# Kernel tuning notes

Measured on AMD Instinct MI355X. Metric: run time of the kernel, lower is better.

The kernel has to match this reference:

```python
import jax, jax.numpy as jnp
import numpy as np

N = 8192       # nodes
E = 262144     # edges per graph view (avg degree 32)
D_IN = 200     # input feature dim
D = 100        # hidden dim
H = 2          # GAT heads (concat=False -> mean over heads)
K = 25         # nearest_neighbor in DHGLayer
A_H = 50       # Attention module hidden dim
LRELU = 0.2
BN_EPS = 1e-5


def _bn_eval(x, gamma, beta):
    # BatchNorm1d in eval mode with running_mean=0, running_var=1 (as initialized)
    return x * (gamma / jnp.sqrt(1.0 + BN_EPS)) + beta


def _gat(x, src, dst, W, att_src, att_dst, bias):
    # PyG GATConv: heads=H, concat=False (head mean), self-loops added, eval (no dropout)
    n = x.shape[0]
    xp = (x @ W).reshape(n, H, D)                          # (n, H, D)
    loop = jnp.arange(n, dtype=src.dtype)
    s = jnp.concatenate([src, loop])
    d = jnp.concatenate([dst, loop])
    a_s = jnp.einsum('nhc,hc->nh', xp, att_src)
    a_d = jnp.einsum('nhc,hc->nh', xp, att_dst)
    e = jax.nn.leaky_relu(a_s[s] + a_d[d], LRELU)          # (E+n, H)
    m = jax.ops.segment_max(e, d, num_segments=n)
    w = jnp.exp(e - m[d])
    z = jax.ops.segment_sum(w, d, num_segments=n)
    alpha = w / z[d]
    out = jax.ops.segment_sum(alpha[:, :, None] * xp[s], d, num_segments=n)
    return out.mean(axis=1) + bias                          # (n, D)


def _dhg(x, Wkk, bkk, w1, b1, fcW, fcb):
    # DHGLayer at ite=1: only the kNN hyperedge branch is active
    # (wu_knn=1 <= ite < wu_kmeans=2 = wu_struct=2). EdgeConv over a single
    # hyperedge degenerates to identity (softmax over one element).
    nrm = jnp.maximum(jnp.linalg.norm(x, axis=1, keepdims=True), 1e-12)
    xn = x / nrm
    sim = jax.lax.stop_gradient(xn @ xn.T)                 # cosine sim, used only for topk indices
    _, idx = jax.lax.top_k(sim, K)                         # (n, K)
    region = x[idx]                                        # (n, K, D) gather
    # Transform: grouped Conv1d(K, K*K, D) -> per-node KxK mixing weights -> softmax -> mix
    mult = jax.nn.softmax(jnp.einsum('nkd,kjd->nkj', region, Wkk) + bkk, axis=-1)
    tf = jnp.einsum('nkj,njd->nkd', mult, region)          # (n, K, D)
    pooled = jnp.einsum('nkd,k->nd', tf, w1) + b1          # Conv1d(K, 1, 1) pooling
    return jax.nn.relu(pooled @ fcW + fcb)                 # GraphConvolution fc + ReLU


def _atten(x, W1, b1, g, b, W2, b2):
    h = jax.nn.sigmoid(_bn_eval(x @ W1 + b1, g, b))
    return h @ W2 + b2                                     # (n, 1)


def _encoder(inputx, edge_index, fea_edge_index,
             g1_W, g1_as, g1_ad, g1_b, g2_W, g2_as, g2_ad, g2_b,
             g3_W, g3_as, g3_ad, g3_b, g4_W, g4_as, g4_ad, g4_b,
             bn_g, bn_b, bn1_g, bn1_b,
             d1_Wkk, d1_bkk, d1_w1, d1_b1, d1_fcW, d1_fcb,
             d2_Wkk, d2_bkk, d2_w1, d2_b1, d2_fcW, d2_fcb,
             a1_W1, a1_b1, a1_g, a1_bb, a1_W2, a1_b2,
             a2_W1, a2_b1, a2_g, a2_bb, a2_W2, a2_b2):
    fs, fd = fea_edge_index[0], fea_edge_index[1]
    es, ed = edge_index[0], edge_index[1]
    feax1 = jax.nn.relu(_bn_eval(_gat(inputx, fs, fd, g1_W, g1_as, g1_ad, g1_b), bn_g, bn_b))
    x1 = jax.nn.relu(_bn_eval(_gat(inputx, es, ed, g2_W, g2_as, g2_ad, g2_b), bn1_g, bn1_b))
    feax1 = _dhg(feax1, d1_Wkk, d1_bkk, d1_w1, d1_b1, d1_fcW, d1_fcb)
    feax2 = _gat(feax1, fs, fd, g3_W, g3_as, g3_ad, g3_b)
    x1 = _dhg(x1, d2_Wkk, d2_bkk, d2_w1, d2_b1, d2_fcW, d2_fcb)
    x2 = _gat(x1, es, ed, g4_W, g4_as, g4_ad, g4_b)
    att1 = _atten(feax2, a1_W1, a1_b1, a1_g, a1_bb, a1_W2, a1_b2)
    att2 = _atten(x2, a2_W1, a2_b1, a2_g, a2_bb, a2_W2, a2_b2)
    att = jax.nn.softmax(jnp.concatenate([att1, att2], axis=1), axis=1)
    return att[:, :1] * feax2 + att[:, 1:] * x2            # (N, D)


def setup_inputs() -> dict:
    key = jax.random.key(0)
    kit = iter(jax.random.split(key, 64))
    nrm = lambda shape, scale: jax.random.normal(next(kit), shape, dtype=jnp.float32) * scale
    inp = {}
    inp['inputx'] = nrm((N, D_IN), 1.0)
    inp['edge_index'] = jax.random.randint(next(kit), (2, E), 0, N)
    inp['fea_edge_index'] = jax.random.randint(next(kit), (2, E), 0, N)
    inp['edge_list'] = jax.random.randint(next(kit), (N, K), 0, N)  # unused at ite=1
    for name, din in (('g1', D_IN), ('g2', D_IN), ('g3', D), ('g4', D)):
        inp[name + '_W'] = nrm((din, H * D), din ** -0.5)
        inp[name + '_as'] = nrm((H, D), D ** -0.5)
        inp[name + '_ad'] = nrm((H, D), D ** -0.5)
        inp[name + '_b'] = jnp.zeros((D,), jnp.float32)
    inp['bn_g'] = jnp.ones((D,), jnp.float32)
    inp['bn_b'] = jnp.zeros((D,), jnp.float32)
    inp['bn1_g'] = jnp.ones((D,), jnp.float32)
    inp['bn1_b'] = jnp.zeros((D,), jnp.float32)
    for name in ('d1', 'd2'):
        inp[name + '_Wkk'] = nrm((K, K, D), D ** -0.5)
        inp[name + '_bkk'] = jnp.zeros((K, K), jnp.float32)
        inp[name + '_w1'] = nrm((K,), K ** -0.5)
        inp[name + '_b1'] = jnp.zeros((1,), jnp.float32)
        inp[name + '_fcW'] = nrm((D, D), D ** -0.5)
        inp[name + '_fcb'] = jnp.zeros((D,), jnp.float32)
    for name in ('a1', 'a2'):
        inp[name + '_W1'] = nrm((D, A_H), D ** -0.5)
        inp[name + '_b1'] = jnp.zeros((A_H,), jnp.float32)
        inp[name + '_g'] = jnp.ones((A_H,), jnp.float32)
        inp[name + '_bb'] = jnp.zeros((A_H,), jnp.float32)
        inp[name + '_W2'] = nrm((A_H, 1), A_H ** -0.5)
        inp[name + '_b2'] = jnp.zeros((1,), jnp.float32)
    return inp


def reference(inputx, edge_index, fea_edge_index, edge_list,
              g1_W, g1_as, g1_ad, g1_b, g2_W, g2_as, g2_ad, g2_b,
              g3_W, g3_as, g3_ad, g3_b, g4_W, g4_as, g4_ad, g4_b,
              bn_g, bn_b, bn1_g, bn1_b,
              d1_Wkk, d1_bkk, d1_w1, d1_b1, d1_fcW, d1_fcb,
              d2_Wkk, d2_bkk, d2_w1, d2_b1, d2_fcW, d2_fcb,
              a1_W1, a1_b1, a1_g, a1_bb, a1_W2, a1_b2,
              a2_W1, a2_b1, a2_g, a2_bb, a2_W2, a2_b2):
    # edge_list is ignored: structured-neighbor branch is not warmed up at ite=1
    return _encoder(inputx, edge_index, fea_edge_index,
                    g1_W, g1_as, g1_ad, g1_b, g2_W, g2_as, g2_ad, g2_b,
                    g3_W, g3_as, g3_ad, g3_b, g4_W, g4_as, g4_ad, g4_b,
                    bn_g, bn_b, bn1_g, bn1_b,
                    d1_Wkk, d1_bkk, d1_w1, d1_b1, d1_fcW, d1_fcb,
                    d2_Wkk, d2_bkk, d2_w1, d2_b1, d2_fcW, d2_fcb,
                    a1_W1, a1_b1, a1_g, a1_bb, a1_W2, a1_b2,
                    a2_W1, a2_b1, a2_g, a2_bb, a2_W2, a2_b2)
```

## Files before the change

### kernel.cpp

```cpp
#include <hip/hip_runtime.h>
#include <math.h>

#define NN 8192
#define EE 262144
#define KNN 25
#define INIT_COLS 1024
#define CAP 768
#define INF INFINITY

typedef unsigned int u32;
typedef unsigned long long u64;

__device__ __forceinline__ float lrelu02(float x){ return x > 0.f ? x : 0.2f*x; }
__device__ __forceinline__ u32 fkey(float f){ u32 b = __float_as_uint(f); return b ^ (u32)(((int)b >> 31) | (int)0x80000000); }

__global__ __launch_bounds__(256) void k_count(const int* __restrict__ dst, int* __restrict__ deg) {
  int e = blockIdx.x*256 + threadIdx.x;
  if (e < EE) atomicAdd(&deg[dst[e]], 1);
}

__global__ __launch_bounds__(1024) void k_scan(const int* __restrict__ deg, int* __restrict__ rowptr) {
  __shared__ int lds[1024];
  int t = threadIdx.x;
  int v[8]; int s = 0;
#pragma unroll
  for (int i=0;i<8;i++){ v[i] = deg[t*8+i]; s += v[i]; }
  lds[t] = s; __syncthreads();
  for (int off=1; off<1024; off<<=1) {
    int x = (t>=off)? lds[t-off] : 0;
    __syncthreads();
    lds[t] += x;
    __syncthreads();
  }
  int base = (t==0)? 0 : lds[t-1];
  if (t==0) rowptr[0] = 0;
  int run = base;
#pragma unroll
  for (int i=0;i<8;i++){ run += v[i]; rowptr[t*8+i+1] = run; }
}

__global__ __launch_bounds__(256) void k_scatter(const int* __restrict__ src, const int* __restrict__ dst,
                          const int* __restrict__ rowptr, int* __restrict__ cursor,
                          int* __restrict__ csr) {
  int e = blockIdx.x*256 + threadIdx.x;
  if (e < EE) {
    int d = dst[e];
    int p = rowptr[d] + atomicAdd(&cursor[d], 1);
    csr[p] = src[e];
  }
}

__global__ __launch_bounds__(256) void k_gemm_small(const float* __restrict__ A, const float* __restrict__ B,
                                                    float* __restrict__ C, int Ncols, int Kdim) {
  __shared__ float Al[50][65];
  __shared__ float Bl[50][65];
  int t = threadIdx.x;
  int tr = t >> 4, tc = t & 15;
  int r0 = blockIdx.x * 64, c0 = blockIdx.y * 64;
  float acc[4][4] = {};
  for (int kc = 0; kc < Kdim; kc += 50) {
    for (int fl = t; fl < 64*50; fl += 256) {
      int m = fl / 50, k = fl - m*50;
      Al[k][m] = A[(long)(r0+m)*Kdim + kc + k];
    }
    for (int fl = t; fl < 50*64; fl += 256) {
      int k = fl >> 6, c = fl & 63;
      int cg = c0 + c;
      Bl[k][c] = (cg < Ncols) ? B[(long)(kc+k)*Ncols + cg] : 0.f;
    }
    __syncthreads();
    for (int k = 0; k < 50; k++) {
      float a_[4], b_[4];
#pragma unroll
      for (int i=0;i<4;i++) a_[i] = Al[k][tr*4+i];
#pragma unroll
      for (int j=0;j<4;j++) b_[j] = Bl[k][tc*4+j];
#pragma unroll
      for (int i=0;i<4;i++)
#pragma unroll
        for (int j=0;j<4;j++) acc[i][j] += a_[i]*b_[j];
    }
    __syncthreads();
  }
#pragma unroll
  for (int i=0;i<4;i++){
    int r = r0 + tr*4 + i;
#pragma unroll
    for (int j=0;j<4;j++){
      int c = c0 + tc*4 + j;
      if (c < Ncols) C[(long)r*Ncols + c] = acc[i][j];
    }
  }
}

__global__ __launch_bounds__(256) void k_gat_coef(const float* __restrict__ xp, const float* __restrict__ as_w,
                                                  const float* __restrict__ ad_w, float* __restrict__ asb,
                                                  float* __restrict__ adb) {
  int g = blockIdx.x*256 + threadIdx.x;
  int n = g >> 2, q = g & 3;
  int h = q >> 1, sd = q & 1;
  const float4* xr = (const float4*)(xp + (long)n*200 + h*100);
  const float4* wr = (const float4*)((sd ? ad_w : as_w) + h*100);
  float acc = 0.f;
#pragma unroll
  for (int q4=0;q4<25;q4++){
    float4 xv = xr[q4], wv = wr[q4];
    acc += xv.x*wv.x + xv.y*wv.y + xv.z*wv.z + xv.w*wv.w;
  }
  (sd ? adb : asb)[n*2 + h] = acc;
}

__global__ __launch_bounds__(256) void k_gat_agg(const float* __restrict__ xp, const float* __restrict__ asb,
                                                 const float* __restrict__ adb, const int* __restrict__ rowptr,
                                                 const int* __restrict__ csr, const float* __restrict__ bias,
                                                 const float* __restrict__ bng, const float* __restrict__ bnb,
                                                 int bnrelu, float* __restrict__ out) {
  __shared__ int esrc[256];
  __shared__ float ew0[256], ew1[256];
  __shared__ float red[2][4];
  __shared__ float ohead[200];
  int i = blockIdx.x, t = threadIdx.x;
  int lane = t & 63, wv = t >> 6;
  int beg = rowptr[i];
  int deg = rowptr[i+1] - beg;
  float ad0 = adb[i*2+0], ad1 = adb[i*2+1];
  float m0 = -INF, m1 = -INF, z0 = 0.f, z1 = 0.f, acc = 0.f;
  int h = (t >= 100) ? 1 : 0;
  int tot = deg + 1;
  for (int base = 0; base < tot; base += 256) {
    int cnt = min(256, tot - base);
    int j = base + t;
    float e0 = -INF, e1 = -INF; int s = i;
    if (t < cnt) {
      if (j < deg) s = csr[beg + j];
      float as0 = asb[s*2+0], as1 = asb[s*2+1];
      e0 = lrelu02(as0 + ad0);
      e1 = lrelu02(as1 + ad1);
    }
    esrc[t] = s;
    float r0v = e0, r1v = e1;
    for (int off=32; off; off>>=1){ r0v = fmaxf(r0v, __shfl_xor(r0v,off)); r1v = fmaxf(r1v, __shfl_xor(r1v,off)); }
    if (lane == 0){ red[0][wv] = r0v; red[1][wv] = r1v; }
    __syncthreads();
    float nm0 = fmaxf(m0, fmaxf(fmaxf(red[0][0],red[0][1]), fmaxf(red[0][2],red[0][3])));
    float nm1 = fmaxf(m1, fmaxf(fmaxf(red[1][0],red[1][1]), fmaxf(red[1][2],red[1][3])));
    float w0 = (t<cnt)? expf(e0-nm0) : 0.f;
    float w1e = (t<cnt)? expf(e1-nm1) : 0.f;
    ew0[t] = w0; ew1[t] = w1e;
    float s0 = w0, s1 = w1e;
    for (int off=32; off; off>>=1){ s0 += __shfl_xor(s0,off); s1 += __shfl_xor(s1,off); }
    __syncthreads();
    if (lane == 0){ red[0][wv] = s0; red[1][wv] = s1; }
    __syncthreads();
    float cs0 = red[0][0]+red[0][1]+red[0][2]+red[0][3];
    float cs1 = red[1][0]+red[1][1]+red[1][2]+red[1][3];
    float rf0 = expf(m0 - nm0);
    float rf1 = expf(m1 - nm1);
    z0 = z0*rf0 + cs0; z1 = z1*rf1 + cs1;
    m0 = nm0; m1 = nm1;
    if (t < 200) {
      acc *= (h==0) ? rf0 : rf1;
      const float* ew = (h==0) ? ew0 : ew1;
      for (int jj = 0; jj < cnt; jj++) {
        acc += ew[jj] * xp[(long)esrc[jj]*200 + t];
      }
    }
    __syncthreads();
  }
  if (t < 200) ohead[t] = acc / ((h==0) ? z0 : z1);
  __syncthreads();
  if (t < 100) {
    float v = 0.5f*(ohead[t] + ohead[100+t]) + bias[t];
    if (bnrelu) {
      v = v * (bng[t]*rsqrtf(1.f+1e-5f)) + bnb[t];
      v = fmaxf(v, 0.f);
    }
    out[(long)i*100 + t] = v;
  }
}

__global__ __launch_bounds__(256) void k_norm(const float* __restrict__ x, float* __restrict__ xnT) {
  int w = threadIdx.x >> 6, lane = threadIdx.x & 63;
  long n = blockIdx.x*4 + w;
  float a = x[n*100 + lane];
  float b = (lane < 36) ? x[n*100 + 64 + lane] : 0.f;
  float ss = a*a + b*b;
  for (int off=32; off; off>>=1) ss += __shfl_xor(ss, off);
  float sc = 1.f / fmaxf(sqrtf(ss), 1e-12f);
  xnT[(long)lane*NN + n] = a*sc;
  if (lane < 36) xnT[(long)(64+lane)*NN + n] = b*sc;
}

__global__ __launch_bounds__(256) void k_sim(const float* __restrict__ xnT, float* __restrict__ simbuf) {
  __shared__ float Al[50][132];
  __shared__ float Bl[50][132];
  int t = threadIdx.x;
  int tr = t >> 4, tc = t & 15;
  int r0 = blockIdx.x * 128;
  int cb = blockIdx.y * 128;
  float acc[8][8] = {};
  for (int kc = 0; kc < 100; kc += 50) {
    for (int fl = t; fl < 50*128; fl += 256) {
      int k = fl >> 7, m = fl & 127;
      const float* src = xnT + (long)(kc+k)*NN;
      Al[k][m] = src[r0 + m];
      Bl[k][m] = src[cb + m];
    }
    __syncthreads();
    for (int k = 0; k < 50; k++) {
      float4 a0 = *(const float4*)&Al[k][4*tr];
      float4 a1 = *(const float4*)&Al[k][4*tr + 64];
      float4 b0 = *(const float4*)&Bl[k][4*tc];
      float4 b1 = *(const float4*)&Bl[k][4*tc + 64];
      float a_[8] = {a0.x,a0.y,a0.z,a0.w,a1.x,a1.y,a1.z,a1.w};
      float b_[8] = {b0.x,b0.y,b0.z,b0.w,b1.x,b1.y,b1.z,b1.w};
#pragma unroll
      for (int i=0;i<8;i++)
#pragma unroll
        for (int j=0;j<8;j++) acc[i][j] += a_[i]*b_[j];
    }
    __syncthreads();
  }
#pragma unroll
  for (int i=0;i<8;i++){
    long r = r0 + ((i<4) ? (4*tr + i) : (64 + 4*tr + i - 4));
    float* crow = simbuf + r*(long)INIT_COLS + cb;
    float4 o0 = make_float4(acc[i][0],acc[i][1],acc[i][2],acc[i][3]);
    float4 o1 = make_float4(acc[i][4],acc[i][5],acc[i][6],acc[i][7]);
    *(float4*)&crow[4*tc]      = o0;
    *(float4*)&crow[64 + 4*tc] = o1;
  }
}

__global__ __launch_bounds__(256) void k_sim_f(const float* __restrict__ xnT, const u32* __restrict__ thr,
                                               int* __restrict__ cnt, u64* __restrict__ candbuf, int cbase) {
  __shared__ float Al[50][132];
  __shared__ float Bl[50][132];
  int t = threadIdx.x;
  int tr = t >> 4, tc = t & 15;
  int r0 = blockIdx.x * 128;
  int cb = blockIdx.y * 128;
  float acc[8][8] = {};
  for (int kc = 0; kc < 100; kc += 50) {
    for (int fl = t; fl < 50*128; fl += 256) {
      int k = fl >> 7, m = fl & 127;
      const float* src = xnT + (long)(kc+k)*NN;
      Al[k][m] = src[r0 + m];
      Bl[k][m] = src[cbase + cb + m];
    }
    __syncthreads();
    for (int k = 0; k < 50; k++) {
      float4 a0 = *(const float4*)&Al[k][4*tr];
      float4 a1 = *(const float4*)&Al[k][4*tr + 64];
      float4 b0 = *(const float4*)&Bl[k][4*tc];
      float4 b1 = *(const float4*)&Bl[k][4*tc + 64];
      float a_[8] = {a0.x,a0.y,a0.z,a0.w,a1.x,a1.y,a1.z,a1.w};
      float b_[8] = {b0.x,b0.y,b0.z,b0.w,b1.x,b1.y,b1.z,b1.w};
#pragma unroll
      for (int i=0;i<8;i++)
#pragma unroll
        for (int j=0;j<8;j++) acc[i][j] += a_[i]*b_[j];
    }
    __syncthreads();
  }
  int sub = t & 15;
#pragma unroll
  for (int i=0;i<8;i++){
    int r = r0 + ((i<4) ? (4*tr + i) : (64 + 4*tr + i - 4));
    u32 T = thr[r];
    unsigned m8 = 0;
#pragma unroll
    for (int j=0;j<8;j++) if (fkey(acc[i][j]) > T) m8 |= 1u<<j;
    int c_lane = __popc(m8);
    int pre = c_lane;
#pragma unroll
    for (int off=1; off<16; off<<=1){ int o = __shfl_up(pre, off, 16); if (sub >= off) pre += o; }
    int tot = __shfl(pre, 15, 16);
    if (tot > 0){
      int base = 0;
      if (sub == 15) base = atomicAdd(&cnt[r], tot);
      base = __shfl(base, 15, 16);
      int p = base + pre - c_lane;
#pragma unroll
      for (int j=0;j<8;j++) if (m8 & (1u<<j)){
        if (p < CAP){
          int c = cbase + cb + ((j<4) ? (4*tc + j) : (64 + 4*tc + j - 4));
          candbuf[(long)r*CAP + p] = ((u64)fkey(acc[i][j]) << 32) | (u32)(0xFFFFFFFFu - (u32)c);
        }
        p++;
      }
    }
  }
}

__global__ __launch_bounds__(256) void k_topk_sel(const float* __restrict__ simbuf,
                                                  u64* __restrict__ candu, u32* __restrict__ thr) {
  __shared__ int hist[256];
  __shared__ int scr2[2];
  __shared__ int cgt, ceq;
  __shared__ u64 win[32];
  __shared__ u32 tie[INIT_COLS];
  int row = blockIdx.x, t = threadIdx.x, lane = t & 63, w = t >> 6;
  const float* srow = simbuf + (long)row*INIT_COLS;
  u32 kk[4]; int col[4];
  {
    int c0 = 4*t;
    float4 f = *(const float4*)&srow[c0];
    kk[0] = fkey(f.x); col[0] = c0;
    kk[1] = fkey(f.y); col[1] = c0+1;
    kk[2] = fkey(f.z); col[2] = c0+2;
    kk[3] = fkey(f.w); col[3] = c0+3;
  }
  u32 prefix = 0; int base_gt = 0;
#pragma unroll
  for (int lvl = 0; lvl < 4; lvl++) {
    int shift = 24 - 8*lvl;
    hist[t] = 0;
    if (lvl == 0 && t == 0) { cgt = 0; ceq = 0; }
    __syncthreads();
    u32 mhi = (lvl == 0) ? 0u : (0xFFFFFFFFu << (32 - 8*lvl));
#pragma unroll
    for (int i = 0; i < 4; i++)
      if ((kk[i] & mhi) == (prefix & mhi)) atomicAdd(&hist[(kk[i] >> shift) & 0xFF], 1);
    __syncthreads();
    if (w == 0) {
      int h0 = hist[4*lane], h1 = hist[4*lane+1], h2 = hist[4*lane+2], h3 = hist[4*lane+3];
      int s = h0 + h1 + h2 + h3;
      int acc = s;
      for (int off = 1; off < 64; off <<= 1) {
        int o = __shfl_down(acc, off);
        if (lane + off < 64) acc += o;
      }
      int T = base_gt + (acc - s);
      int b0c = -1; int cumc = T;
      if (cumc < 25 && cumc + h3 >= 25) b0c = 3;
      else { cumc += h3;
        if (cumc < 25 && cumc + h2 >= 25) b0c = 2;
        else { cumc += h2;
          if (cumc < 25 && cumc + h1 >= 25) b0c = 1;
          else { cumc += h1;
            if (cumc < 25 && cumc + h0 >= 25) b0c = 0;
          }
        }
      }
      u64 bal = __ballot(b0c >= 0);
      int ls = __ffsll(bal) - 1;
      int b0 = __shfl(b0c, ls);
      int cum = __shfl(cumc, ls);
      int bl = __shfl(lane, ls);
      if (lane == 0) { scr2[0] = 4*bl + b0; scr2[1] = cum; }
    }
    __syncthreads();
    prefix |= ((u32)scr2[0]) << shift;
    base_gt = scr2[1];
  }
  u32 K25 = prefix;
#pragma unroll
  for (int i = 0; i < 4; i++) {
    if (kk[i] > K25) {
      int p = atomicAdd(&cgt, 1);
      win[p] = ((u64)kk[i] << 32) | (u32)(0xFFFFFFFFu - (u32)col[i]);
    } else if (kk[i] == K25) {
      int p = atomicAdd(&ceq, 1);
      tie[p] = (u32)col[i];
    }
  }
  __syncthreads();
  int wc = cgt, tc = ceq, need = 25 - wc;
  if (tc == need) {
    if (t < need) win[wc + t] = ((u64)K25 << 32) | (u32)(0xFFFFFFFFu - tie[t]);
  } else if (w == 0) {
    for (int sel = 0; sel < need; sel++) {
      u32 m = 0xFFFFFFFFu;
      for (int i = lane; i < tc; i += 64) m = min(m, tie[i]);
      for (int off = 32; off; off >>= 1) m = min(m, (u32)__shfl_xor((int)m, off));
      for (int i = lane; i < tc; i += 64) if (tie[i] == m) tie[i] = 0xFFFFFFFFu;
      if (lane == 0) win[wc + sel] = ((u64)K25 << 32) | (u32)(0xFFFFFFFFu - m);
    }
  }
  __syncthreads();
  if (t < 32) {
    u64 v = (t < 25) ? win[t] : 0ULL;
#pragma unroll
    for (int kb = 2; kb <= 32; kb <<= 1) {
#pragma unroll
      for (int j = kb >> 1; j > 0; j >>= 1) {
        u64 o = __shfl_xor(v, j);
        bool dirAsc = ((t & kb) == 0);
        bool isLow = ((t & j) == 0);
        u64 mn = (v < o) ? v : o;
        u64 mx = (v < o) ? o : v;
        v = (dirAsc == isLow) ? mx : mn;
      }
    }
    if (t < 25) candu[(long)row*25 + t] = v;
  }
  if (t == 0) thr[row] = K25;
}

__global__ __launch_bounds__(256) void k_topk_fmerge(const u64* __restrict__ candu, const int* __restrict__ cnt,
                                                     const u64* __restrict__ candbuf, int* __restrict__ lib) {
  int lane = threadIdx.x & 63;
  int row = blockIdx.x*4 + (threadIdx.x >> 6);
  u64 v = (lane < 25) ? candu[(long)row*25 + lane] : 0ULL;
  int C = cnt[row]; if (C > CAP) C = CAP;
  for (int off = 0; off < C; off += 39) {
    int take = min(39, C - off);
    u64 x = (lane < 25) ? v : ((lane - 25 < take) ? candbuf[(long)row*CAP + off + (lane-25)] : 0ULL);
#pragma unroll
    for (int kb = 2; kb <= 64; kb <<= 1) {
#pragma unroll
      for (int j = kb >> 1; j > 0; j >>= 1) {
        u64 o = __shfl_xor(x, j);
        bool dirAsc = ((lane & kb) == 0);
        bool isLow = ((lane & j) == 0);
        u64 mn = (x < o) ? x : o;
        u64 mx = (x < o) ? o : x;
        x = (dirAsc == isLow) ? mx : mn;
      }
    }
    v = x;
  }
  if (lane < 25) lib[row*KNN + lane] = (int)(0xFFFFFFFFu - (u32)v);
}

__global__ __launch_bounds__(256) void k_dhg_s(const float* __restrict__ x, const int* __restrict__ li,
                                               const float* __restrict__ Wkk, const float* __restrict__ bkk,
                                               const float* __restrict__ w1, float* __restrict__ coefp) {
  __shared__ float Wl[KNN][100];
  __shared__ float bk[KNN];
  __shared__ float w1s;
  int t = threadIdx.x;
  int k = blockIdx.y;
  for (int fl = t; fl < KNN*100; fl += 256) ((float*)Wl)[fl] = Wkk[k*2500 + fl];
  if (t < KNN) bk[t] = bkk[k*KNN + t];
  if (t == 32) w1s = w1[k];
  __syncthreads();
  int n = blockIdx.x*256 + t;
  int id = li[n*KNN + k];
  float4 r4[25];
  const float4* xr = (const float4*)(x + (long)id*100);
#pragma unroll
  for (int q=0;q<25;q++) r4[q] = xr[q];
  float sv[KNN];
  float mx = -INF;
#pragma unroll
  for (int j=0;j<KNN;j++) {
    float acc = bk[j];
#pragma unroll
    for (int q=0;q<25;q++) {
      float4 wvv = *(const float4*)&Wl[j][q*4];
      acc += r4[q].x*wvv.x; acc += r4[q].y*wvv.y; acc += r4[q].z*wvv.z; acc += r4[q].w*wvv.w;
    }
    sv[j] = acc;
    mx = fmaxf(mx, acc);
  }
  float se = 0.f;
#pragma unroll
  for (int j=0;j<KNN;j++){ sv[j] = expf(sv[j]-mx); se += sv[j]; }
  float sc = w1s / se;
#pragma unroll
  for (int j=0;j<KNN;j++) coefp[(long)(k*KNN + j)*NN + n] = sc*sv[j];
}

__global__ __launch_bounds__(256) void k_dhg_reduce(const float* __restrict__ coefp, float* __restrict__ coef) {
  int g = blockIdx.x*256 + threadIdx.x;
  int j = g >> 13;
  int n = g & (NN-1);
  float s = 0.f;
#pragma unroll
  for (int k=0;k<KNN;k++) s += coefp[(long)(k*KNN + j)*NN + n];
  coef[(long)n*KNN + j] = s;
}

__global__ __launch_bounds__(128) void k_dhg_pool(const float* __restrict__ x, const int* __restrict__ li,
                                                  const float* __restrict__ coef, const float* __restrict__ b1,
                                                  const float* __restrict__ fcW, const float* __restrict__ fcb,
                                                  float* __restrict__ out) {
  __shared__ float cf[KNN];
  __shared__ int id[KNN];
  __shared__ float pl[100];
  int n = blockIdx.x; int t = threadIdx.x;
  if (t < KNN) { cf[t] = coef[n*KNN+t]; id[t] = li[n*KNN+t]; }
  __syncthreads();
  if (t < 100) {
    float acc = b1[0];
#pragma unroll
    for (int j=0;j<KNN;j++) acc += cf[j] * x[(long)id[j]*100 + t];
    pl[t] = acc;
  }
  __syncthreads();
  if (t < 100) {
    float o = fcb[t];
    for (int d=0; d<100; d++) o += pl[d] * fcW[d*100 + t];
    out[(long)n*100 + t] = fmaxf(o, 0.f);
  }
}

__global__ __launch_bounds__(128) void k_final(const float* __restrict__ f2b, const float* __restrict__ x2b,
    const float* __restrict__ w1a, const float* __restrict__ b1a, const float* __restrict__ ga, const float* __restrict__ bba,
    const float* __restrict__ w2a, const float* __restrict__ b2a,
    const float* __restrict__ w1b, const float* __restrict__ b1b, const float* __restrict__ gb, const float* __restrict__ bbb,
    const float* __restrict__ w2b, const float* __restrict__ b2b,
    float* __restrict__ outp) {
  __shared__ float f2[100], xr[100], hh[100], att[2];
  int n = blockIdx.x, t = threadIdx.x;
  if (t < 100) { f2[t] = f2b[(long)n*100+t]; xr[t] = x2b[(long)n*100+t]; }
  __syncthreads();
  if (t < 50) {
    float a = b1a[t];
    for (int d=0; d<100; d++) a += f2[d]*w1a[d*50+t];
    a = a*(ga[t]*rsqrtf(1.f+1e-5f)) + bba[t];
    hh[t] = 1.f/(1.f+expf(-a));
  } else if (t >= 64 && t < 114) {
    int jj = t-64;
    float a = b1b[jj];
    for (int d=0; d<100; d++) a += xr[d]*w1b[d*50+jj];
    a = a*(gb[jj]*rsqrtf(1.f+1e-5f)) + bbb[jj];
    hh[50+jj] = 1.f/(1.f+expf(-a));
  }
  __syncthreads();
  {
    int lane = t & 63, w = t >> 6;
    float c = 0.f;
    if (lane < 50) c = hh[w*50 + lane] * (w ? w2b[lane] : w2a[lane]);
    for (int off=32; off; off>>=1) c += __shfl_down(c, off);
    if (lane == 0) att[w] = c + (w ? b2b[0] : b2a[0]);
  }
  __syncthreads();
  if (t < 100) {
    float A1 = att[0], A2 = att[1];
    float mxv = fmaxf(A1, A2);
    float e1 = expf(A1-mxv), e2 = expf(A2-mxv);
    float inv = 1.f/(e1+e2);
    outp[(long)n*100+t] = (e1*inv)*f2[t] + (e2*inv)*xr[t];
  }
}

extern "C" void kernel_launch(void* const* d_in, const int* in_sizes, int n_in,
                              void* d_out, int out_size, void* d_ws, size_t ws_size,
                              hipStream_t stream) {
  (void)in_sizes; (void)n_in; (void)out_size; (void)ws_size;
  const float* inputx = (const float*)d_in[0];
  const int*   ei     = (const int*)d_in[1];
  const int*   fi     = (const int*)d_in[2];
  const float* g1W = (const float*)d_in[4],  *g1as = (const float*)d_in[5],  *g1ad = (const float*)d_in[6],  *g1b = (const float*)d_in[7];
  const float* g2W = (const float*)d_in[8],  *g2as = (const float*)d_in[9],  *g2ad = (const float*)d_in[10], *g2b = (const float*)d_in[11];
  const float* g3W = (const float*)d_in[12], *g3as = (const float*)d_in[13], *g3ad = (const float*)d_in[14], *g3b = (const float*)d_in[15];
  const float* g4W = (const float*)d_in[16], *g4as = (const float*)d_in[17], *g4ad = (const float*)d_in[18], *g4b = (const float*)d_in[19];
  const float* bng = (const float*)d_in[20], *bnb = (const float*)d_in[21];
  const float* bn1g = (const float*)d_in[22], *bn1b = (const float*)d_in[23];
  const float* d1Wkk = (const float*)d_in[24], *d1bkk = (const float*)d_in[25], *d1w1 = (const float*)d_in[26],
             * d1b1 = (const float*)d_in[27], *d1fcW = (const float*)d_in[28], *d1fcb = (const float*)d_in[29];
  const float* d2Wkk = (const float*)d_in[30], *d2bkk = (const float*)d_in[31], *d2w1 = (const float*)d_in[32],
             * d2b1 = (const float*)d_in[33], *d2fcW = (const float*)d_in[34], *d2fcb = (const float*)d_in[35];
  const float* a1W1 = (const float*)d_in[36], *a1b1 = (const float*)d_in[37], *a1g = (const float*)d_in[38],
             * a1bb = (const float*)d_in[39], *a1W2 = (const float*)d_in[40], *a1b2 = (const float*)d_in[41];
  const float* a2W1 = (const float*)d_in[42], *a2b1 = (const float*)d_in[43], *a2g = (const float*)d_in[44],
             * a2bb = (const float*)d_in[45], *a2W2 = (const float*)d_in[46], *a2b2 = (const float*)d_in[47];

  char* wbase = (char*)d_ws; size_t off = 0;
  auto alloc = [&](size_t b)->void*{ off = (off + 255) & ~(size_t)255; void* p = wbase + off; off += b; return p; };
  int* csrEp = (int*)alloc((NN+1)*4);
  int* csrEs = (int*)alloc((size_t)EE*4);
  int* csrFp = (int*)alloc((NN+1)*4);
  int* csrFs = (int*)alloc((size_t)EE*4);
  int* deg   = (int*)alloc(NN*4);
  int* cur   = (int*)alloc(NN*4);
  float* xp    = (float*)alloc((size_t)NN*200*4);
  float* asb   = (float*)alloc((size_t)NN*2*4);
  float* adb   = (float*)alloc((size_t)NN*2*4);
  float* feax1 = (float*)alloc((size_t)NN*100*4);
  float* x1    = (float*)alloc((size_t)NN*100*4);
  float* feax2 = (float*)alloc((size_t)NN*100*4);
  float* x2v   = (float*)alloc((size_t)NN*100*4);
  float* dtmp  = (float*)alloc((size_t)NN*100*4);
  float* xnT   = (float*)alloc((size_t)NN*100*4);
  int*   lib   = (int*)alloc((size_t)NN*KNN*4);
  float* coef  = (float*)alloc((size_t)NN*KNN*4);
  u64*   candu = (u64*)alloc((size_t)NN*KNN*8);
  u32*   thr   = (u32*)alloc((size_t)NN*4);
  int*   cnt   = (int*)alloc((size_t)NN*4);
  size_t ubytes = (size_t)NN*CAP*8;
  char* uregion = (char*)alloc(ubytes);
  float* simbuf  = (float*)uregion;
  u64*   candbuf = (u64*)uregion;
  float* coefp   = (float*)uregion;

  auto buildCSR = [&](const int* e, int* rp, int* cs){
    hipMemsetAsync(deg, 0, NN*4, stream);
    k_count<<<EE/256, 256, 0, stream>>>(e+EE, deg);
    k_scan<<<1, 1024, 0, stream>>>(deg, rp);
    hipMemsetAsync(cur, 0, NN*4, stream);
    k_scatter<<<EE/256, 256, 0, stream>>>(e, e+EE, rp, cur, cs);
  };
  buildCSR(ei, csrEp, csrEs);
  buildCSR(fi, csrFp, csrFs);

  auto GAT = [&](const float* x, int Kdim, const float* W, const float* as_w, const float* ad_w, const float* b,
                 const int* rp, const int* cs, const float* bg, const float* bb, int bnrelu, float* outb){
    k_gemm_small<<<dim3(NN/64, 4), 256, 0, stream>>>(x, W, xp, 200, Kdim);
    k_gat_coef<<<NN*4/256, 256, 0, stream>>>(xp, as_w, ad_w, asb, adb);
    k_gat_agg<<<NN, 256, 0, stream>>>(xp, asb, adb, rp, cs, b, bg, bb, bnrelu, outb);
  };
  auto DHG = [&](const float* x, const float* Wkk, const float* bkk, const float* w1p, const float* b1p,
                 const float* fcW, const float* fcb, float* outb){
    k_norm<<<NN/4, 256, 0, stream>>>(x, xnT);
    k_sim<<<dim3(NN/128, INIT_COLS/128), 256, 0, stream>>>(xnT, simbuf);
    k_topk_sel<<<NN, 256, 0, stream>>>(simbuf, candu, thr);
    hipMemsetAsync(cnt, 0, NN*4, stream);
    k_sim_f<<<dim3(NN/128, (NN-INIT_COLS)/128), 256, 0, stream>>>(xnT, thr, cnt, candbuf, INIT_COLS);
    k_topk_fmerge<<<NN/4, 256, 0, stream>>>(candu, cnt, candbuf, lib);
    k_dhg_s<<<dim3(NN/256, KNN), 256, 0, stream>>>(x, lib, Wkk, bkk, w1p, coefp);
    k_dhg_reduce<<<NN*KNN/256, 256, 0, stream>>>(coefp, coef);
    k_dhg_pool<<<NN, 128, 0, stream>>>(x, lib, coef, b1p, fcW, fcb, outb);
  };

  GAT(inputx, 200, g1W, g1as, g1ad, g1b, csrFp, csrFs, bng,  bnb,  1, feax1);
  GAT(inputx, 200, g2W, g2as, g2ad, g2b, csrEp, csrEs, bn1g, bn1b, 1, x1);
  DHG(feax1, d1Wkk, d1bkk, d1w1, d1b1, d1fcW, d1fcb, dtmp);
  GAT(dtmp, 100, g3W, g3as, g3ad, g3b, csrFp, csrFs, nullptr, nullptr, 0, feax2);
  DHG(x1, d2Wkk, d2bkk, d2w1, d2b1, d2fcW, d2fcb, dtmp);
  GAT(dtmp, 100, g4W, g4as, g4ad, g4b, csrEp, csrEs, nullptr, nullptr, 0, x2v);
  k_final<<<NN, 128, 0, stream>>>(feax2, x2v, a1W1, a1b1, a1g, a1bb, a1W2, a1b2,
                                  a2W1, a2b1, a2g, a2bb, a2W2, a2b2, (float*)d_out);
}
```

Baseline: 1.276 ms.

## Exploit symmetry of cosine similarity to skip lower-triangle tiles in filter pass

The similarity filter kernel now computes only upper-triangle 128x128 tiles (I <= J) and reuses each off-diagonal tile for both row and column candidate emission, using the symmetry of xn·xnᵀ. This roughly halves the GEMM work in the candidate-filtering pass. In exchange, off-diagonal tiles emit extra per-column candidates with per-element atomics, which adds more atomic traffic. The launch grid is presumably sized elsewhere, and the cbase parameter is now unused.

Result: slower. 1.318 ms (+3.2%).

```diff
diff --git a/kernel.cpp b/kernel.cpp
--- a/kernel.cpp
+++ b/kernel.cpp
@@ -5,6 +5,7 @@
 #define EE 262144
 #define KNN 25
 #define INIT_COLS 1024
+#define INIT_BLK (INIT_COLS/128)
 #define CAP 768
 #define INF INFINITY
 
@@ -236,17 +237,20 @@
                                                int* __restrict__ cnt, u64* __restrict__ candbuf, int cbase) {
   __shared__ float Al[50][132];
   __shared__ float Bl[50][132];
+  int I = blockIdx.x;
+  int J = blockIdx.y + INIT_BLK;
+  if (I > J) return;
   int t = threadIdx.x;
   int tr = t >> 4, tc = t & 15;
-  int r0 = blockIdx.x * 128;
-  int cb = blockIdx.y * 128;
+  int r0 = I * 128;
+  int cb = J * 128;
   float acc[8][8] = {};
   for (int kc = 0; kc < 100; kc += 50) {
     for (int fl = t; fl < 50*128; fl += 256) {
       int k = fl >> 7, m = fl & 127;
       const float* src = xnT + (long)(kc+k)*NN;
       Al[k][m] = src[r0 + m];
-      Bl[k][m] = src[cbase + cb + m];
+      Bl[k][m] = src[cb + m];
     }
     __syncthreads();
     for (int k = 0; k < 50; k++) {
@@ -284,13 +288,36 @@
 #pragma unroll
       for (int j=0;j<8;j++) if (m8 & (1u<<j)){
         if (p < CAP){
-          int c = cbase + cb + ((j<4) ? (4*tc + j) : (64 + 4*tc + j - 4));
+          int c = cb + ((j<4) ? (4*tc + j) : (64 + 4*tc + j - 4));
           candbuf[(long)r*CAP + p] = ((u64)fkey(acc[i][j]) << 32) | (u32)(0xFFFFFFFFu - (u32)c);
         }
         p++;
       }
     }
   }
+  if (I >= INIT_BLK && I < J) {
+#pragma unroll
+    for (int j=0;j<8;j++){
+      int c = cb + ((j<4) ? (4*tc + j) : (64 + 4*tc + j - 4));
+      u32 Tc = thr[c];
+      unsigned mi = 0;
+#pragma unroll
+      for (int i=0;i<8;i++) if (fkey(acc[i][j]) > Tc) mi |= 1u<<i;
+      int pc = __popc(mi);
+      if (pc){
+        int p = atomicAdd(&cnt[c], pc);
+#pragma unroll
+        for (int i=0;i<8;i++) if (mi & (1u<<i)){
+          if (p < CAP){
+            int rr = r0 + ((i<4) ? (4*tr + i) : (64 + 4*tr + i - 4));
+            candbuf[(long)c*CAP + p] = ((u64)fkey(acc[i][j]) << 32) | (u32)(0xFFFFFFFFu - (u32)rr);
+          }
+          p++;
+        }
+      }
+    }
+  }
+  (void)cbase;
 }
 
 __global__ __launch_bounds__(256) void k_topk_sel(const float* __restrict__ simbuf,
```
